# Kernel optimization log

Hardware: AMD Instinct MI355X
Metric: run time of the kernel (lower is better)

## Reference

```python
import jax, jax.numpy as jnp
from jax import lax
import numpy as np

B, T = 256, 1024
LSTM_DIMS = [(64, 128), (256, 128), (256, 64)]  # (input, hidden) per layer


def setup_inputs() -> dict:
    key = jax.random.key(0)
    ks = jax.random.split(key, 32)
    s = 0.05
    p = {}
    p["x"] = jax.random.normal(ks[0], (B, 1, T), jnp.float32)
    p["conv_w"] = jax.random.normal(ks[1], (64, 1, 5), jnp.float32) * s  # OIW
    p["conv_b"] = jnp.zeros((64,), jnp.float32)
    for i, (D, H) in enumerate(LSTM_DIMS, 1):
        p[f"w_ih{i}"] = jax.random.normal(ks[3 * i], (2, 4 * H, D), jnp.float32) * s  # [dir, 4H, D]
        p[f"w_hh{i}"] = jax.random.normal(ks[3 * i + 1], (2, 4 * H, H), jnp.float32) * s
        p[f"b{i}"] = jnp.zeros((2, 4 * H), jnp.float32)  # b_ih + b_hh combined (equivalent math)
    fc_dims = [(512, 128), (256, 512), (128, 256), (2, 128)]
    for j, (O, I) in enumerate(fc_dims, 1):
        p[f"fc{j}_w"] = jax.random.normal(ks[12 + 2 * j], (O, I), jnp.float32) * s
        p[f"fc{j}_b"] = jnp.zeros((O,), jnp.float32)
    return p


def _lstm_dir(x, w_ih, w_hh, b, reverse):
    # x: [B,T,D] -> h: [B,T,H]; PyTorch gate order i,f,g,o
    Hh = w_hh.shape[1]
    xs = jnp.swapaxes(x, 0, 1)  # [T,B,D]
    if reverse:
        xs = xs[::-1]
    xw = jnp.einsum('tbd,gd->tbg', xs, w_ih) + b  # precompute input GEMMs: [T,B,4H]

    def step(carry, xw_t):
        h, c = carry
        gates = xw_t + h @ w_hh.T
        i, f, g, o = jnp.split(gates, 4, axis=-1)
        c = jax.nn.sigmoid(f) * c + jax.nn.sigmoid(i) * jnp.tanh(g)
        h = jax.nn.sigmoid(o) * jnp.tanh(c)
        return (h, c), h

    Bx = x.shape[0]
    init = (jnp.zeros((Bx, Hh), x.dtype), jnp.zeros((Bx, Hh), x.dtype))
    _, hs = lax.scan(step, init, xw)
    if reverse:
        hs = hs[::-1]
    return jnp.swapaxes(hs, 0, 1)  # [B,T,H]


def _bilstm(x, w_ih, w_hh, b):
    hf = _lstm_dir(x, w_ih[0], w_hh[0], b[0], False)
    hb = _lstm_dir(x, w_ih[1], w_hh[1], b[1], True)
    return jnp.concatenate([hf, hb], axis=-1)


def reference(x, conv_w, conv_b, w_ih1, w_hh1, b1, w_ih2, w_hh2, b2,
              w_ih3, w_hh3, b3, fc1_w, fc1_b, fc2_w, fc2_b, fc3_w, fc3_b, fc4_w, fc4_b):
    # causal conv: left-pad (k-1)=4, then VALID conv
    xp = jnp.pad(x, ((0, 0), (0, 0), (4, 0)))
    y = lax.conv_general_dilated(xp, conv_w, (1,), 'VALID',
                                 dimension_numbers=('NCH', 'OIH', 'NCH'))
    y = jax.nn.relu(y + conv_b[None, :, None]).transpose(0, 2, 1)  # [B,T,64]
    y = _bilstm(y, w_ih1, w_hh1, b1)  # [B,T,256]
    y = _bilstm(y, w_ih2, w_hh2, b2)  # [B,T,256]
    y = _bilstm(y, w_ih3, w_hh3, b3)  # [B,T,128]
    h = y[:, -1, :]  # [B,128]
    h = jax.nn.relu(h @ fc1_w.T + fc1_b)
    h = jax.nn.relu(h @ fc2_w.T + fc2_b)
    h = jax.nn.relu(h @ fc3_w.T + fc3_b)
    return h @ fc4_w.T + fc4_b  # [B,2]
```

## Files before the change

kernel.cpp:

```cpp
#include <hip/hip_runtime.h>
#include <hip/hip_bf16.h>
#include <cstdint>
#include <cstddef>

#define B_ALL 256
#define T_SZ  1024

typedef __attribute__((ext_vector_type(8))) _Float16  halfx8;
typedef __attribute__((ext_vector_type(4))) _Float16  halfx4;
typedef __attribute__((ext_vector_type(4))) float     f32x4;

__device__ __forceinline__ float sig_(float x) {
    return __builtin_amdgcn_rcpf(1.0f + __expf(-x));
}
__device__ __forceinline__ float tanh_(float x) {
    float ax = fabsf(x);
    float e  = __expf(-2.0f * ax);
    float t  = (1.0f - e) * __builtin_amdgcn_rcpf(1.0f + e);
    return copysignf(t, x);
}

__device__ __forceinline__ void bar_lgkm() {
    asm volatile("s_waitcnt lgkmcnt(0)\n\ts_barrier" ::: "memory");
}

__global__ void conv_relu_kernel(const float* __restrict__ x, const float* __restrict__ w,
                                 const float* __restrict__ bias, _Float16* __restrict__ out,
                                 int bg0)
{
    int c  = threadIdx.x & 63;
    int tq = threadIdx.x >> 6;
    int t  = blockIdx.x * 4 + tq;
    int b  = blockIdx.y;
    const float* xb = x + (size_t)(bg0 + b) * T_SZ;
    float s = bias[c];
#pragma unroll
    for (int k = 0; k < 5; ++k) {
        int ti = t - 4 + k;
        float xv = (ti >= 0) ? xb[ti] : 0.0f;
        s = fmaf(w[c * 5 + k], xv, s);
    }
    out[((size_t)b * T_SZ + t) * 64 + c] = (_Float16)fmaxf(s, 0.0f);
}

template <int H, int NW, bool WRITE_Y>
__global__ __launch_bounds__(512, 1) void fused_step(
    const _Float16* __restrict__ xwR, const float* __restrict__ w_hh,
    _Float16* __restrict__ y, float* __restrict__ lastOut,
    float* __restrict__ Hst, float* __restrict__ Cst,
    int Bg, int Tc, int lg, int step0, int zeroInit, int writeLast,
    int nRecBlocks, int ndirRec,
    const _Float16* __restrict__ A, const float* __restrict__ W,
    const float* __restrict__ bias, _Float16* __restrict__ xwOut,
    int K, int N, int t0p, int MT, int NT, int nProjB, int totTiles)
{
    __shared__ __align__(16) char smem[32768];
    const int tid = threadIdx.x;
    const int w   = tid >> 6;
    const int l   = tid & 63;
    const int l15 = l & 15;
    const int q4  = l >> 4;

    if ((int)blockIdx.x < nRecBlocks) {
        constexpr int FH  = 4 * H;
        constexpr int KT  = H / 32;
        constexpr int NCH = H / 8;
        int rb  = blockIdx.x;
        int dir = (ndirRec == 2) ? (rb & 1) : 0;
        int bt  = (ndirRec == 2) ? (rb >> 1) : rb;
        int brow = bt * 4 + q4;
        int hh   = w * 16 + l15;

        _Float16* hb = (_Float16*)smem;
        auto hAddr = [&](int p, int row, int ch) -> _Float16* {
            return hb + ((((p * 16 + row) * NCH) + (ch ^ (row & (NCH - 1)))) << 3);
        };
        for (int i = tid; i < 2 * 16 * H; i += 512) hb[i] = (_Float16)0.f;
        __syncthreads();

        halfx8 wf[4][KT];
        float creg = 0.f;
        if (w < NW) {
            const float* wbase = w_hh + (size_t)dir * FH * H;
#pragma unroll
            for (int gate = 0; gate < 4; ++gate) {
                const float* wrow = wbase + (size_t)(gate * H + hh) * H;
#pragma unroll
                for (int kt = 0; kt < KT; ++kt) {
                    const float* src = wrow + kt * 32 + q4 * 8;
                    float4 a = *(const float4*)(src);
                    float4 b = *(const float4*)(src + 4);
                    halfx8 v;
                    v[0] = (_Float16)a.x; v[1] = (_Float16)a.y; v[2] = (_Float16)a.z; v[3] = (_Float16)a.w;
                    v[4] = (_Float16)b.x; v[5] = (_Float16)b.y; v[6] = (_Float16)b.z; v[7] = (_Float16)b.w;
                    wf[gate][kt] = v;
                }
            }
            float hv = 0.f;
            if (!zeroInit) {
                hv   = Hst[((size_t)dir * Bg + brow) * H + hh];
                creg = Cst[((size_t)dir * Bg + brow) * H + hh];
            }
            hAddr(0, q4 * 4, hh >> 3)[hh & 7] = (_Float16)hv;
        }
        const _Float16* xb = xwR + (size_t)dir * Tc * Bg * FH + (size_t)brow * FH + hh * 4;
        const size_t xstride = (size_t)Bg * FH;

        halfx4 pf0, pf1, pf2, pf3;
        if (w < NW) {
            pf0 = *(const halfx4*)(xb);
            pf1 = *(const halfx4*)(xb + xstride);
            pf2 = *(const halfx4*)(xb + 2 * xstride);
            pf3 = *(const halfx4*)(xb + 3 * xstride);
        }
        __syncthreads();

        auto step = [&](int sl, int P, halfx4 xv) {
            const int t = dir ? (T_SZ - 1 - (step0 + sl)) : (step0 + sl);
            halfx8 af[KT];
#pragma unroll
            for (int kt = 0; kt < KT; ++kt)
                af[kt] = *(const halfx8*)hAddr(P, l15, kt * 4 + q4);
            float g4[4];
#pragma unroll
            for (int gate = 0; gate < 4; ++gate) {
                f32x4 a = {0.f, 0.f, 0.f, 0.f};
#pragma unroll
                for (int kt = 0; kt < KT; ++kt)
                    a = __builtin_amdgcn_mfma_f32_16x16x32_f16(af[kt], wf[gate][kt], a, 0, 0, 0);
                g4[gate] = a[0] + (float)xv[gate];
            }
            float iv = fminf(fmaxf(g4[0], -25.f), 25.f);
            float fv = fminf(fmaxf(g4[1], -25.f), 25.f);
            float gv = fminf(fmaxf(g4[2], -12.f), 12.f);
            float ov = fminf(fmaxf(g4[3], -25.f), 25.f);
            float Af = 1.f + __expf(-fv);
            float Bi = 1.f + __expf(-iv);
            float G  = __expf(2.f * gv);
            float Gp = G + 1.f, Gm = G - 1.f;
            float num = fmaf(creg * Bi, Gp, Af * Gm);
            float cn  = num * __builtin_amdgcn_rcpf(Af * Bi * Gp);
            creg = cn;
            float cc = fminf(fmaxf(cn, -25.f), 25.f);
            float E  = __expf(2.f * cc);
            float hv = (E - 1.f) * __builtin_amdgcn_rcpf((1.f + __expf(-ov)) * (E + 1.f));
            hAddr(1 - P, q4 * 4, hh >> 3)[hh & 7] = (_Float16)hv;
            if (WRITE_Y) {
                y[((size_t)brow * T_SZ + t) * (2 * H) + dir * H + hh] = (_Float16)hv;
            } else if (writeLast && sl == Tc - 1) {
                lastOut[brow * 128 + hh] = hv;
            }
            if (sl == Tc - 1) {
                Hst[((size_t)dir * Bg + brow) * H + hh] = hv;
                Cst[((size_t)dir * Bg + brow) * H + hh] = cn;
            }
        };

        for (int sl4 = 0; sl4 < Tc; sl4 += 4) {
            if (w < NW) {
                step(sl4 + 0, 0, pf0);
                if (sl4 + 4 < Tc) pf0 = *(const halfx4*)(xb + (size_t)(sl4 + 4) * xstride);
            }
            bar_lgkm();
            if (w < NW) {
                step(sl4 + 1, 1, pf1);
                if (sl4 + 5 < Tc) pf1 = *(const halfx4*)(xb + (size_t)(sl4 + 5) * xstride);
            }
            bar_lgkm();
            if (w < NW) {
                step(sl4 + 2, 0, pf2);
                if (sl4 + 6 < Tc) pf2 = *(const halfx4*)(xb + (size_t)(sl4 + 6) * xstride);
            }
            bar_lgkm();
            if (w < NW) {
                step(sl4 + 3, 1, pf3);
                if (sl4 + 7 < Tc) pf3 = *(const halfx4*)(xb + (size_t)(sl4 + 7) * xstride);
            }
            bar_lgkm();
        }
    } else {
        const int Tcp = 1 << lg;
        const int H4  = N >> 2;
        int pb = blockIdx.x - nRecBlocks;

        for (int tile = pb; tile < totTiles; tile += nProjB) {
            int mi   = tile % MT;
            int rest = tile / MT;
            int ni   = rest % NT;
            int dirp = rest / NT;
            const float* Wd = W + (size_t)dirp * N * K;
            const float* bd = bias + (size_t)dirp * N;
            _Float16*    od = xwOut + (size_t)dirp * Tcp * Bg * N;

            _Float16 (*As)[40] = (_Float16(*)[40])smem;
            _Float16 (*Ws)[40] = (_Float16(*)[40])(smem + 10240);

            const int m0 = mi * 128;
            const int n0 = ni * 128;
            const int wm = (w & 1) * 64;
            const int wn = (w >> 1) * 32;

            f32x4 acc[4][2];
#pragma unroll
            for (int i = 0; i < 4; i++)
#pragma unroll
                for (int j = 0; j < 2; j++) acc[i][j] = (f32x4){0.f, 0.f, 0.f, 0.f};

            for (int k0 = 0; k0 < K; k0 += 32) {
                {
                    int row = tid >> 2;
                    int ko  = (tid & 3) * 8;
                    int m   = m0 + row;
                    int bA  = m >> lg, tl = m & (Tcp - 1);
                    int t   = dirp ? (T_SZ - 1 - (t0p + tl)) : (t0p + tl);
                    const _Float16* src = A + ((size_t)bA * T_SZ + t) * K + k0 + ko;
                    *(halfx8*)&As[row][ko] = *(const halfx8*)src;
                }
#pragma unroll
                for (int pass = 0; pass < 2; ++pass) {
                    int c2  = tid + pass * 512;
                    int row = c2 >> 3;
                    int ko  = (c2 & 7) * 4;
                    int n_o = n0 + row;
                    int nr  = (n_o & 3) * H4 + (n_o >> 2);
                    float4 f = *(const float4*)&Wd[(size_t)nr * K + k0 + ko];
                    halfx4 v;
                    v[0] = (_Float16)f.x; v[1] = (_Float16)f.y; v[2] = (_Float16)f.z; v[3] = (_Float16)f.w;
                    *(halfx4*)&Ws[row][ko] = v;
                }
                bar_lgkm();
                halfx8 af[4], bfr[2];
#pragma unroll
                for (int i = 0; i < 4; i++) af[i]  = *(const halfx8*)&As[wm + i * 16 + l15][q4 * 8];
#pragma unroll
                for (int j = 0; j < 2; j++) bfr[j] = *(const halfx8*)&Ws[wn + j * 16 + l15][q4 * 8];
#pragma unroll
                for (int i = 0; i < 4; i++)
#pragma unroll
                    for (int j = 0; j < 2; j++)
                        acc[i][j] = __builtin_amdgcn_mfma_f32_16x16x32_f16(af[i], bfr[j], acc[i][j], 0, 0, 0);
                bar_lgkm();
            }

            _Float16 (*Ct)[128] = (_Float16(*)[128])smem;
#pragma unroll
            for (int i = 0; i < 4; i++) {
#pragma unroll
                for (int j = 0; j < 2; j++) {
                    int o_l = wn + j * 16 + l15;
                    int n_o = n0 + o_l;
                    float bi = bd[(n_o & 3) * H4 + (n_o >> 2)];
#pragma unroll
                    for (int r = 0; r < 4; r++)
                        Ct[wm + i * 16 + q4 * 4 + r][o_l] = (_Float16)(acc[i][j][r] + bi);
                }
            }
            bar_lgkm();
            {
                int row = tid >> 2;
                int seg = tid & 3;
                int m   = m0 + row;
                int bO  = m >> lg, tl = m & (Tcp - 1);
                _Float16* dst = od + ((size_t)tl * Bg + bO) * N + n0 + seg * 32;
                const _Float16* srcp = &Ct[row][seg * 32];
#pragma unroll
                for (int u = 0; u < 4; ++u)
                    *(halfx8*)(dst + u * 8) = *(const halfx8*)(srcp + u * 8);
            }
            bar_lgkm();
        }
    }
}

__global__ __launch_bounds__(256) void lstm3_bwd_kernel(
    const _Float16* __restrict__ y2, const float* __restrict__ w_ih3,
    const float* __restrict__ b3, float* __restrict__ H3)
{
    int b = blockIdx.x, g = threadIdx.x;
    __shared__ float xr[256];
    __shared__ float gsh[256];
    xr[g] = (float)y2[((size_t)b * T_SZ + (T_SZ - 1)) * 256 + g];
    __syncthreads();
    const float* wr = w_ih3 + (size_t)256 * 256 + (size_t)g * 256;
    float acc = b3[256 + g];
#pragma unroll 4
    for (int k = 0; k < 256; k++) acc = fmaf(wr[k], xr[k], acc);
    gsh[g] = acc;
    __syncthreads();
    if (g < 64) {
        float iv = gsh[g], gv = gsh[128 + g], ov = gsh[192 + g];
        float ct = sig_(iv) * tanh_(gv);
        float hv = sig_(ov) * tanh_(ct);
        H3[b * 128 + 64 + g] = hv;
    }
}

__global__ void fc_kernel(const float* __restrict__ in, const float* __restrict__ W,
                          const float* __restrict__ bias, float* __restrict__ out,
                          int K, int N, int doRelu)
{
    int b = blockIdx.x;
    int g = threadIdx.x;
    extern __shared__ float xr[];
    for (int i = g; i < K; i += blockDim.x) xr[i] = in[(size_t)b * K + i];
    __syncthreads();
    if (g < N) {
        const float* wr = W + (size_t)g * K;
        float acc = bias[g];
        for (int k = 0; k < K; k++) acc = fmaf(wr[k], xr[k], acc);
        if (doRelu) acc = fmaxf(acc, 0.f);
        out[(size_t)b * N + g] = acc;
    }
}

extern "C" void kernel_launch(void* const* d_in, const int* in_sizes, int n_in,
                              void* d_out, int out_size, void* d_ws, size_t ws_size,
                              hipStream_t stream)
{
    (void)in_sizes; (void)n_in; (void)out_size;
    const float* x      = (const float*)d_in[0];
    const float* conv_w = (const float*)d_in[1];
    const float* conv_b = (const float*)d_in[2];
    const float* w_ih1  = (const float*)d_in[3];
    const float* w_hh1  = (const float*)d_in[4];
    const float* b1     = (const float*)d_in[5];
    const float* w_ih2  = (const float*)d_in[6];
    const float* w_hh2  = (const float*)d_in[7];
    const float* b2     = (const float*)d_in[8];
    const float* w_ih3  = (const float*)d_in[9];
    const float* w_hh3  = (const float*)d_in[10];
    const float* b3     = (const float*)d_in[11];
    const float* fc1_w  = (const float*)d_in[12];
    const float* fc1_b  = (const float*)d_in[13];
    const float* fc2_w  = (const float*)d_in[14];
    const float* fc2_b  = (const float*)d_in[15];
    const float* fc3_w  = (const float*)d_in[16];
    const float* fc3_b  = (const float*)d_in[17];
    const float* fc4_w  = (const float*)d_in[18];
    const float* fc4_b  = (const float*)d_in[19];
    float* out = (float*)d_out;
    char*  base = (char*)d_ws;

    const size_t MB = 1ull << 20;

    auto need = [&](int s, int tc) -> size_t {
        size_t Bg = B_ALL / s;
        size_t YB = Bg * T_SZ * 256 * 2;
        size_t XW = (size_t)tc * Bg * 512 * 2 * 2;
        return 2 * YB + 2 * XW + 2 * MB;
    };

    int S = 8;
    for (int s : {1, 2, 4, 8}) {
        if (need(s, 32) <= ws_size) { S = s; break; }
    }
    int Tc = 32;
    while (Tc < 256 && need(S, Tc * 2) <= ws_size) Tc <<= 1;
    int lg = 0; while ((1 << lg) < Tc) lg++;
    int NC = T_SZ / Tc;

    int Bg = B_ALL / S;
    size_t YB  = (size_t)Bg * T_SZ * 256 * 2;
    size_t XWB = (size_t)Tc * Bg * 512 * 2 * 2;
    _Float16* Y1 = (_Float16*)base;
    _Float16* Y2 = (_Float16*)(base + YB);
    _Float16* X1 = Y2;
    _Float16* XW[2] = { (_Float16*)(base + 2 * YB), (_Float16*)(base + 2 * YB + XWB) };
    float* sm  = (float*)(base + 2 * YB + 2 * XWB);
    float* Hs = sm;
    float* Cs = Hs + 2 * Bg * 128;
    float* H3 = Cs + 2 * Bg * 128;
    float* F1 = H3 + Bg * 128;
    float* F2 = F1 + Bg * 512;
    float* F3 = F2 + Bg * 256;

    int MT = Bg * Tc / 128;

    for (int sp = 0; sp < S; ++sp) {
        int bg0 = sp * Bg;

        conv_relu_kernel<<<dim3(T_SZ / 4, Bg), 256, 0, stream>>>(x, conv_w, conv_b, X1, bg0);

        {
            int NT = 4, ndir = 2, Kl = 64, Nn = 512;
            int nRec  = (Bg / 4) * ndir;
            int nProjB = 256 - nRec; if (nProjB < 64) nProjB = 64;
            int totT  = MT * NT * ndir;
            fused_step<128, 8, true><<<256, 512, 0, stream>>>(
                XW[0], w_hh1, Y1, H3, Hs, Cs, Bg, Tc, lg, 0, 1, 0, 0, ndir,
                X1, w_ih1, b1, XW[0], Kl, Nn, 0, MT, NT, 256, totT);
            int par = 0;
            for (int ci = 0; ci < NC; ++ci) {
                int last = (ci == NC - 1);
                int grid = nRec + (last ? 0 : nProjB);
                fused_step<128, 8, true><<<grid, 512, 0, stream>>>(
                    XW[par], w_hh1, Y1, H3, Hs, Cs, Bg, Tc, lg, ci * Tc, ci == 0, 0, nRec, ndir,
                    X1, w_ih1, b1, XW[1 - par], Kl, Nn, (ci + 1) * Tc, MT, NT, nProjB, totT);
                par ^= 1;
            }
        }
        {
            int NT = 4, ndir = 2, Kl = 256, Nn = 512;
            int nRec  = (Bg / 4) * ndir;
            int nProjB = 256 - nRec; if (nProjB < 64) nProjB = 64;
            int totT  = MT * NT * ndir;
            fused_step<128, 8, true><<<256, 512, 0, stream>>>(
                XW[0], w_hh2, Y2, H3, Hs, Cs, Bg, Tc, lg, 0, 1, 0, 0, ndir,
                Y1, w_ih2, b2, XW[0], Kl, Nn, 0, MT, NT, 256, totT);
            int par = 0;
            for (int ci = 0; ci < NC; ++ci) {
                int last = (ci == NC - 1);
                int grid = nRec + (last ? 0 : nProjB);
                fused_step<128, 8, true><<<grid, 512, 0, stream>>>(
                    XW[par], w_hh2, Y2, H3, Hs, Cs, Bg, Tc, lg, ci * Tc, ci == 0, 0, nRec, ndir,
                    Y1, w_ih2, b2, XW[1 - par], Kl, Nn, (ci + 1) * Tc, MT, NT, nProjB, totT);
                par ^= 1;
            }
        }
        {
            int NT = 2, ndir = 1, Kl = 256, Nn = 256;
            int nRec  = (Bg / 4) * ndir;
            int nProjB = 256 - nRec; if (nProjB < 64) nProjB = 64;
            int totT  = MT * NT * ndir;
            fused_step<64, 4, false><<<256, 512, 0, stream>>>(
                XW[0], w_hh3, nullptr, H3, Hs, Cs, Bg, Tc, lg, 0, 1, 0, 0, ndir,
                Y2, w_ih3, b3, XW[0], Kl, Nn, 0, MT, NT, 256, totT);
            int par = 0;
            for (int ci = 0; ci < NC; ++ci) {
                int last = (ci == NC - 1);
                int grid = nRec + (last ? 0 : nProjB);
                fused_step<64, 4, false><<<grid, 512, 0, stream>>>(
                    XW[par], w_hh3, nullptr, H3, Hs, Cs, Bg, Tc, lg, ci * Tc, ci == 0, last, nRec, ndir,
                    Y2, w_ih3, b3, XW[1 - par], Kl, Nn, (ci + 1) * Tc, MT, NT, nProjB, totT);
                par ^= 1;
            }
        }
        lstm3_bwd_kernel<<<Bg, 256, 0, stream>>>(Y2, w_ih3, b3, H3);

        fc_kernel<<<Bg, 512, 128 * 4, stream>>>(H3, fc1_w, fc1_b, F1, 128, 512, 1);
        fc_kernel<<<Bg, 256, 512 * 4, stream>>>(F1, fc2_w, fc2_b, F2, 512, 256, 1);
        fc_kernel<<<Bg, 128, 256 * 4, stream>>>(F2, fc3_w, fc3_b, F3, 256, 128, 1);
        fc_kernel<<<Bg, 64, 128 * 4, stream>>>(F3, fc4_w, fc4_b, out + (size_t)bg0 * 2, 128, 2, 0);
    }
}
```

Before: 3.643 ms.

## Process multiple hidden groups per wave in recurrent LSTM step for H=128

Generalizes the recurrent step so each wave handles NHG hidden-unit groups, and launches layers 1 and 2 with 4 active waves instead of 8, so each wave computes two 16-column groups. The MFMA K-loop is split into two independent accumulators to shorten dependency chains. The aim is fewer waves taking part in each per-timestep barrier and more independent MFMA work per wave for latency hiding. The cost is doubled weight-fragment registers per wave, which raises register pressure, plus longer serial work per wave between barriers.

```diff
diff --git a/kernel.cpp b/kernel.cpp
--- a/kernel.cpp
+++ b/kernel.cpp
@@ -65,11 +65,14 @@
         constexpr int FH  = 4 * H;
         constexpr int KT  = H / 32;
         constexpr int NCH = H / 8;
+        constexpr int NHG = H / (16 * NW);
         int rb  = blockIdx.x;
         int dir = (ndirRec == 2) ? (rb & 1) : 0;
         int bt  = (ndirRec == 2) ? (rb >> 1) : rb;
         int brow = bt * 4 + q4;
-        int hh   = w * 16 + l15;
+        int hhg[NHG];
+#pragma unroll
+        for (int hg = 0; hg < NHG; ++hg) hhg[hg] = (w + hg * NW) * 16 + l15;
 
         _Float16* hb = (_Float16*)smem;
         auto hAddr = [&](int p, int row, int ch) -> _Float16* {
@@ -78,103 +81,135 @@
         for (int i = tid; i < 2 * 16 * H; i += 512) hb[i] = (_Float16)0.f;
         __syncthreads();
 
-        halfx8 wf[4][KT];
-        float creg = 0.f;
+        halfx8 wf[NHG][4][KT];
+        float creg[NHG];
+#pragma unroll
+        for (int hg = 0; hg < NHG; ++hg) creg[hg] = 0.f;
         if (w < NW) {
             const float* wbase = w_hh + (size_t)dir * FH * H;
 #pragma unroll
-            for (int gate = 0; gate < 4; ++gate) {
-                const float* wrow = wbase + (size_t)(gate * H + hh) * H;
-#pragma unroll
-                for (int kt = 0; kt < KT; ++kt) {
-                    const float* src = wrow + kt * 32 + q4 * 8;
-                    float4 a = *(const float4*)(src);
-                    float4 b = *(const float4*)(src + 4);
-                    halfx8 v;
-                    v[0] = (_Float16)a.x; v[1] = (_Float16)a.y; v[2] = (_Float16)a.z; v[3] = (_Float16)a.w;
-                    v[4] = (_Float16)b.x; v[5] = (_Float16)b.y; v[6] = (_Float16)b.z; v[7] = (_Float16)b.w;
-                    wf[gate][kt] = v;
-                }
-            }
-            float hv = 0.f;
-            if (!zeroInit) {
-                hv   = Hst[((size_t)dir * Bg + brow) * H + hh];
-                creg = Cst[((size_t)dir * Bg + brow) * H + hh];
-            }
-            hAddr(0, q4 * 4, hh >> 3)[hh & 7] = (_Float16)hv;
-        }
-        const _Float16* xb = xwR + (size_t)dir * Tc * Bg * FH + (size_t)brow * FH + hh * 4;
+            for (int hg = 0; hg < NHG; ++hg) {
+#pragma unroll
+                for (int gate = 0; gate < 4; ++gate) {
+                    const float* wrow = wbase + (size_t)(gate * H + hhg[hg]) * H;
+#pragma unroll
+                    for (int kt = 0; kt < KT; ++kt) {
+                        const float* src = wrow + kt * 32 + q4 * 8;
+                        float4 a = *(const float4*)(src);
+                        float4 b = *(const float4*)(src + 4);
+                        halfx8 v;
+                        v[0] = (_Float16)a.x; v[1] = (_Float16)a.y; v[2] = (_Float16)a.z; v[3] = (_Float16)a.w;
+                        v[4] = (_Float16)b.x; v[5] = (_Float16)b.y; v[6] = (_Float16)b.z; v[7] = (_Float16)b.w;
+                        wf[hg][gate][kt] = v;
+                    }
+                }
+                float hv = 0.f;
+                if (!zeroInit) {
+                    hv       = Hst[((size_t)dir * Bg + brow) * H + hhg[hg]];
+                    creg[hg] = Cst[((size_t)dir * Bg + brow) * H + hhg[hg]];
+                }
+                hAddr(0, q4 * 4, hhg[hg] >> 3)[hhg[hg] & 7] = (_Float16)hv;
+            }
+        }
+        const _Float16* xbp[NHG];
+#pragma unroll
+        for (int hg = 0; hg < NHG; ++hg)
+            xbp[hg] = xwR + (size_t)dir * Tc * Bg * FH + (size_t)brow * FH + hhg[hg] * 4;
         const size_t xstride = (size_t)Bg * FH;
 
-        halfx4 pf0, pf1, pf2, pf3;
+        halfx4 pf[4][NHG];
         if (w < NW) {
-            pf0 = *(const halfx4*)(xb);
-            pf1 = *(const halfx4*)(xb + xstride);
-            pf2 = *(const halfx4*)(xb + 2 * xstride);
-            pf3 = *(const halfx4*)(xb + 3 * xstride);
+#pragma unroll
+            for (int j = 0; j < 4; ++j)
+#pragma unroll
+                for (int hg = 0; hg < NHG; ++hg)
+                    pf[j][hg] = *(const halfx4*)(xbp[hg] + (size_t)j * xstride);
         }
         __syncthreads();
 
-        auto step = [&](int sl, int P, halfx4 xv) {
+        auto step = [&](int sl, int P, const halfx4* xv) {
             const int t = dir ? (T_SZ - 1 - (step0 + sl)) : (step0 + sl);
             halfx8 af[KT];
 #pragma unroll
             for (int kt = 0; kt < KT; ++kt)
                 af[kt] = *(const halfx8*)hAddr(P, l15, kt * 4 + q4);
-            float g4[4];
-#pragma unroll
-            for (int gate = 0; gate < 4; ++gate) {
-                f32x4 a = {0.f, 0.f, 0.f, 0.f};
-#pragma unroll
-                for (int kt = 0; kt < KT; ++kt)
-                    a = __builtin_amdgcn_mfma_f32_16x16x32_f16(af[kt], wf[gate][kt], a, 0, 0, 0);
-                g4[gate] = a[0] + (float)xv[gate];
-            }
-            float iv = fminf(fmaxf(g4[0], -25.f), 25.f);
-            float fv = fminf(fmaxf(g4[1], -25.f), 25.f);
-            float gv = fminf(fmaxf(g4[2], -12.f), 12.f);
-            float ov = fminf(fmaxf(g4[3], -25.f), 25.f);
-            float Af = 1.f + __expf(-fv);
-            float Bi = 1.f + __expf(-iv);
-            float G  = __expf(2.f * gv);
-            float Gp = G + 1.f, Gm = G - 1.f;
-            float num = fmaf(creg * Bi, Gp, Af * Gm);
-            float cn  = num * __builtin_amdgcn_rcpf(Af * Bi * Gp);
-            creg = cn;
-            float cc = fminf(fmaxf(cn, -25.f), 25.f);
-            float E  = __expf(2.f * cc);
-            float hv = (E - 1.f) * __builtin_amdgcn_rcpf((1.f + __expf(-ov)) * (E + 1.f));
-            hAddr(1 - P, q4 * 4, hh >> 3)[hh & 7] = (_Float16)hv;
-            if (WRITE_Y) {
-                y[((size_t)brow * T_SZ + t) * (2 * H) + dir * H + hh] = (_Float16)hv;
-            } else if (writeLast && sl == Tc - 1) {
-                lastOut[brow * 128 + hh] = hv;
-            }
-            if (sl == Tc - 1) {
-                Hst[((size_t)dir * Bg + brow) * H + hh] = hv;
-                Cst[((size_t)dir * Bg + brow) * H + hh] = cn;
+#pragma unroll
+            for (int hg = 0; hg < NHG; ++hg) {
+                float g4[4];
+#pragma unroll
+                for (int gate = 0; gate < 4; ++gate) {
+                    f32x4 a0 = {0.f, 0.f, 0.f, 0.f};
+                    f32x4 a1 = {0.f, 0.f, 0.f, 0.f};
+#pragma unroll
+                    for (int kt = 0; kt < KT / 2; ++kt)
+                        a0 = __builtin_amdgcn_mfma_f32_16x16x32_f16(af[kt], wf[hg][gate][kt], a0, 0, 0, 0);
+#pragma unroll
+                    for (int kt = KT / 2; kt < KT; ++kt)
+                        a1 = __builtin_amdgcn_mfma_f32_16x16x32_f16(af[kt], wf[hg][gate][kt], a1, 0, 0, 0);
+                    g4[gate] = a0[0] + a1[0] + (float)xv[hg][gate];
+                }
+                float iv = fminf(fmaxf(g4[0], -25.f), 25.f);
+                float fv = fminf(fmaxf(g4[1], -25.f), 25.f);
+                float gv = fminf(fmaxf(g4[2], -12.f), 12.f);
+                float ov = fminf(fmaxf(g4[3], -25.f), 25.f);
+                float Af = 1.f + __expf(-fv);
+                float Bi = 1.f + __expf(-iv);
+                float G  = __expf(2.f * gv);
+                float Gp = G + 1.f, Gm = G - 1.f;
+                float num = fmaf(creg[hg] * Bi, Gp, Af * Gm);
+                float cn  = num * __builtin_amdgcn_rcpf(Af * Bi * Gp);
+                creg[hg] = cn;
+                float cc = fminf(fmaxf(cn, -25.f), 25.f);
+                float E  = __expf(2.f * cc);
+                float hv = (E - 1.f) * __builtin_amdgcn_rcpf((1.f + __expf(-ov)) * (E + 1.f));
+                hAddr(1 - P, q4 * 4, hhg[hg] >> 3)[hhg[hg] & 7] = (_Float16)hv;
+                if (WRITE_Y) {
+                    y[((size_t)brow * T_SZ + t) * (2 * H) + dir * H + hhg[hg]] = (_Float16)hv;
+                } else if (writeLast && sl == Tc - 1) {
+                    lastOut[brow * 128 + hhg[hg]] = hv;
+                }
+                if (sl == Tc - 1) {
+                    Hst[((size_t)dir * Bg + brow) * H + hhg[hg]] = hv;
+                    Cst[((size_t)dir * Bg + brow) * H + hhg[hg]] = cn;
+                }
             }
         };
 
         for (int sl4 = 0; sl4 < Tc; sl4 += 4) {
             if (w < NW) {
-                step(sl4 + 0, 0, pf0);
-                if (sl4 + 4 < Tc) pf0 = *(const halfx4*)(xb + (size_t)(sl4 + 4) * xstride);
+                step(sl4 + 0, 0, pf[0]);
+                if (sl4 + 4 < Tc) {
+#pragma unroll
+                    for (int hg = 0; hg < NHG; ++hg)
+                        pf[0][hg] = *(const halfx4*)(xbp[hg] + (size_t)(sl4 + 4) * xstride);
+                }
             }
             bar_lgkm();
             if (w < NW) {
-                step(sl4 + 1, 1, pf1);
-                if (sl4 + 5 < Tc) pf1 = *(const halfx4*)(xb + (size_t)(sl4 + 5) * xstride);
+                step(sl4 + 1, 1, pf[1]);
+                if (sl4 + 5 < Tc) {
+#pragma unroll
+                    for (int hg = 0; hg < NHG; ++hg)
+                        pf[1][hg] = *(const halfx4*)(xbp[hg] + (size_t)(sl4 + 5) * xstride);
+                }
             }
             bar_lgkm();
             if (w < NW) {
-                step(sl4 + 2, 0, pf2);
-                if (sl4 + 6 < Tc) pf2 = *(const halfx4*)(xb + (size_t)(sl4 + 6) * xstride);
+                step(sl4 + 2, 0, pf[2]);
+                if (sl4 + 6 < Tc) {
+#pragma unroll
+                    for (int hg = 0; hg < NHG; ++hg)
+                        pf[2][hg] = *(const halfx4*)(xbp[hg] + (size_t)(sl4 + 6) * xstride);
+                }
             }
             bar_lgkm();
             if (w < NW) {
-                step(sl4 + 3, 1, pf3);
-                if (sl4 + 7 < Tc) pf3 = *(const halfx4*)(xb + (size_t)(sl4 + 7) * xstride);
+                step(sl4 + 3, 1, pf[3]);
+                if (sl4 + 7 < Tc) {
+#pragma unroll
+                    for (int hg = 0; hg < NHG; ++hg)
+                        pf[3][hg] = *(const halfx4*)(xbp[hg] + (size_t)(sl4 + 7) * xstride);
+                }
             }
             bar_lgkm();
         }
@@ -386,14 +421,14 @@
             int nRec  = (Bg / 4) * ndir;
             int nProjB = 256 - nRec; if (nProjB < 64) nProjB = 64;
             int totT  = MT * NT * ndir;
-            fused_step<128, 8, true><<<256, 512, 0, stream>>>(
+            fused_step<128, 4, true><<<256, 512, 0, stream>>>(
                 XW[0], w_hh1, Y1, H3, Hs, Cs, Bg, Tc, lg, 0, 1, 0, 0, ndir,
                 X1, w_ih1, b1, XW[0], Kl, Nn, 0, MT, NT, 256, totT);
             int par = 0;
             for (int ci = 0; ci < NC; ++ci) {
                 int last = (ci == NC - 1);
                 int grid = nRec + (last ? 0 : nProjB);
-                fused_step<128, 8, true><<<grid, 512, 0, stream>>>(
+                fused_step<128, 4, true><<<grid, 512, 0, stream>>>(
                     XW[par], w_hh1, Y1, H3, Hs, Cs, Bg, Tc, lg, ci * Tc, ci == 0, 0, nRec, ndir,
                     X1, w_ih1, b1, XW[1 - par], Kl, Nn, (ci + 1) * Tc, MT, NT, nProjB, totT);
                 par ^= 1;
@@ -404,14 +439,14 @@
             int nRec  = (Bg / 4) * ndir;
             int nProjB = 256 - nRec; if (nProjB < 64) nProjB = 64;
             int totT  = MT * NT * ndir;
-            fused_step<128, 8, true><<<256, 512, 0, stream>>>(
+            fused_step<128, 4, true><<<256, 512, 0, stream>>>(
                 XW[0], w_hh2, Y2, H3, Hs, Cs, Bg, Tc, lg, 0, 1, 0, 0, ndir,
                 Y1, w_ih2, b2, XW[0], Kl, Nn, 0, MT, NT, 256, totT);
             int par = 0;
             for (int ci = 0; ci < NC; ++ci) {
                 int last = (ci == NC - 1);
                 int grid = nRec + (last ? 0 : nProjB);
-                fused_step<128, 8, true><<<grid, 512, 0, stream>>>(
+                fused_step<128, 4, true><<<grid, 512, 0, stream>>>(
                     XW[par], w_hh2, Y2, H3, Hs, Cs, Bg, Tc, lg, ci * Tc, ci == 0, 0, nRec, ndir,
                     Y1, w_ih2, b2, XW[1 - par], Kl, Nn, (ci + 1) * Tc, MT, NT, nProjB, totT);
                 par ^= 1;
```

After: 4.683 ms. 28.6% more time.
